# Kernel optimization log

Hardware: AMD Instinct MI355X
Metric: run time of the kernel (lower is better)

The kernel has to match this reference:

```python
import jax, jax.numpy as jnp
import numpy as np

D, H, W = 160, 192, 160


def _grid_sample_3d(vol, grid):
    """torch F.grid_sample (3D, bilinear/trilinear, padding='zeros', align_corners=False).
    vol: [B,C,D,H,W]; grid: [B,Do,Ho,Wo,3], last dim ordered (x,y,z) in [-1,1]."""
    B, C, Dv, Hv, Wv = vol.shape
    x, y, z = grid[..., 0], grid[..., 1], grid[..., 2]
    # align_corners=False unnormalization
    ix = ((x + 1.0) * Wv - 1.0) * 0.5
    iy = ((y + 1.0) * Hv - 1.0) * 0.5
    iz = ((z + 1.0) * Dv - 1.0) * 0.5
    fx, fy, fz = jnp.floor(ix), jnp.floor(iy), jnp.floor(iz)
    wx, wy, wz = ix - fx, iy - fy, iz - fz
    ix0, iy0, iz0 = fx.astype(jnp.int32), fy.astype(jnp.int32), fz.astype(jnp.int32)
    vol_flat = vol.reshape(B, C, Dv * Hv * Wv)
    out_sp = x.shape[1:]  # (Do, Ho, Wo)

    def gather(zi, yi, xi):
        inb = ((zi >= 0) & (zi < Dv) & (yi >= 0) & (yi < Hv) & (xi >= 0) & (xi < Wv))
        lin = ((jnp.clip(zi, 0, Dv - 1) * Hv + jnp.clip(yi, 0, Hv - 1)) * Wv
               + jnp.clip(xi, 0, Wv - 1)).reshape(B, -1)
        vals = jax.vmap(lambda v, i: v[:, i])(vol_flat, lin)  # [B,C,N]
        return vals.reshape((B, C) + out_sp) * inb[:, None].astype(vol.dtype)

    out = jnp.zeros((B, C) + tuple(out_sp), vol.dtype)
    # fixed 8-corner trilinear accumulation
    for dz, wz_ in ((0, 1.0 - wz), (1, wz)):
        for dy, wy_ in ((0, 1.0 - wy), (1, wy)):
            for dx, wx_ in ((0, 1.0 - wx), (1, wx)):
                w = (wz_ * wy_ * wx_)[:, None]  # [B,1,Do,Ho,Wo]
                out = out + w * gather(iz0 + dz, iy0 + dy, ix0 + dx)
    return out


def _voxel_grid():
    gd, gh, gw = jnp.meshgrid(jnp.arange(D, dtype=jnp.float32),
                              jnp.arange(H, dtype=jnp.float32),
                              jnp.arange(W, dtype=jnp.float32), indexing='ij')
    return jnp.stack([gd, gh, gw])[None]  # [1,3,D,H,W], channels (d,h,w)


def _to_xyz(t):
    # [B,3,D,H,W] channels (d,h,w) -> [B,D,H,W,3] channels (x,y,z)
    return jnp.moveaxis(t, 1, -1)[..., ::-1]


def setup_inputs() -> dict:
    key = jax.random.key(0)
    k1, k2, k3 = jax.random.split(key, 3)
    src = jax.random.normal(k1, (1, 1, D, H, W), dtype=jnp.float32)
    flow1 = jax.random.normal(k2, (1, 3, D, H, W), dtype=jnp.float32)
    flow2 = jax.random.normal(k3, (1, 3, D, H, W), dtype=jnp.float32)
    range_flow = jnp.float32(0.4)
    return {"src": src, "flow1": flow1, "flow2": flow2, "range_flow": range_flow}


def reference(src, flow1, flow2, range_flow):
    grid = _voxel_grid()  # voxel-coordinate identity grid
    # NOTE: grid2 is intentionally NOT normalized to [-1,1] (faithful to source quirk)
    grid2 = _to_xyz(grid + flow2 * range_flow)
    flow1_warped = _grid_sample_3d(flow1, grid2)
    out_flow = flow1_warped + flow2
    denom = jnp.array([D - 1, H - 1, W - 1], jnp.float32).reshape(1, 3, 1, 1, 1)
    new_locs_total = 2.0 * ((grid + out_flow * range_flow) / denom - 0.5)
    deform_2_img = _grid_sample_3d(src, _to_xyz(new_locs_total))
    return deform_2_img, out_flow
```

## Files before the change

kernel.cpp:

```cpp
#include <hip/hip_runtime.h>

constexpr int Dv = 160, Hv = 192, Wv = 160;
constexpr int NN = Dv * Hv * Wv;

constexpr int TW = 32, TH = 8, TD = 8;
constexpr int SX = 40, SY = 13, SZ = 13;
constexpr int SLEN = SX * SY * SZ;
constexpr int SVEC = SLEN / 4;
constexpr int SITER = (SVEC + 255) / 256;
constexpr int SPAD = SITER * 256 * 4;

__device__ __forceinline__ void tri3_rare(const float* __restrict__ v,
                                          float gx, float gy, float gz,
                                          float& o0, float& o1, float& o2) {
  o0 = 0.0f; o1 = 0.0f; o2 = 0.0f;
  float ix = ((gx + 1.0f) * (float)Wv - 1.0f) * 0.5f;
  float iy = ((gy + 1.0f) * (float)Hv - 1.0f) * 0.5f;
  float iz = ((gz + 1.0f) * (float)Dv - 1.0f) * 0.5f;
  float fx = floorf(ix), fy = floorf(iy), fz = floorf(iz);
  int x0 = (int)fx, y0 = (int)fy, z0 = (int)fz;
  if (x0 < -1 || x0 >= Wv || y0 < -1 || y0 >= Hv || z0 < -1 || z0 >= Dv)
    return;
  float wx = ix - fx, wy = iy - fy, wz = iz - fz;
#pragma unroll
  for (int c = 0; c < 8; ++c) {
    const int dz = (c >> 2) & 1, dy = (c >> 1) & 1, dx = c & 1;
    int zi = z0 + dz, yi = y0 + dy, xi = x0 + dx;
    if ((unsigned)zi < (unsigned)Dv && (unsigned)yi < (unsigned)Hv &&
        (unsigned)xi < (unsigned)Wv) {
      float wgt = (dz ? wz : 1.0f - wz) * (dy ? wy : 1.0f - wy) *
                  (dx ? wx : 1.0f - wx);
      int lin = (zi * Hv + yi) * Wv + xi;
      o0 += wgt * v[lin];
      o1 += wgt * v[NN + lin];
      o2 += wgt * v[2 * NN + lin];
    }
  }
}

__global__ __launch_bounds__(256)
void st_tiled_kernel(const float* __restrict__ src,
                     const float* __restrict__ flow1,
                     const float* __restrict__ flow2,
                     const float* __restrict__ rfp,
                     float* __restrict__ out) {
  __shared__ float tile[SPAD];

  const int tid = threadIdx.x;
  const int bx0 = blockIdx.x * TW;
  const int by0 = blockIdx.y * TH;
  const int bz0 = blockIdx.z * TD;
  const float rf = rfp[0];

  const int lx = tid & 7;
  const int ly = (tid >> 3) & 7;
  const int lz = tid >> 6;
  const int w0 = bx0 + lx * 4;
  const int h = by0 + ly;

  float4 f2d4[2], f2h4[2], f2w4[2];
#pragma unroll
  for (int s = 0; s < 2; ++s) {
    int d = bz0 + 2 * lz + s;
    int idx = (d * Hv + h) * Wv + w0;
    f2d4[s] = *(const float4*)(flow2 + idx);
    f2h4[s] = *(const float4*)(flow2 + NN + idx);
    f2w4[s] = *(const float4*)(flow2 + 2 * NN + idx);
  }

  const int bxo = bx0 - 4, byo = by0 - 2, bzo = bz0 - 2;
#pragma unroll
  for (int i = 0; i < SITER; ++i) {
    int t = tid + i * 256;
    int tt = (i == SITER - 1) ? min(t, SVEC - 1) : t;
    int e = tt * 4;
    int tz = e / (SY * SX);
    int r = e - tz * (SY * SX);
    int ty = r / SX;
    int tx = r - ty * SX;
    int gx = min(max(bxo + tx, 0), Wv - 4);
    int gy = min(max(byo + ty, 0), Hv - 1);
    int gz = min(max(bzo + tz, 0), Dv - 1);
    int g = (gz * Hv + gy) * Wv + gx;
    __builtin_amdgcn_global_load_lds(
        (const __attribute__((address_space(1))) void*)(src + g),
        (__attribute__((address_space(3))) void*)(tile + e), 16, 0, 0);
  }
  __syncthreads();

  const float hf = (float)h;
  constexpr float KX = (float)Wv / (float)(Wv - 1);
  constexpr float KY = (float)Hv / (float)(Hv - 1);
  constexpr float KZ = (float)Dv / (float)(Dv - 1);

#pragma unroll
  for (int s = 0; s < 2; ++s) {
    const int d = bz0 + 2 * lz + s;
    const float df = (float)d;
    const int idx = (d * Hv + h) * Wv + w0;

    float4 def, ofd4, ofh4, ofw4;
#pragma unroll
    for (int j = 0; j < 4; ++j) {
      const float wf = (float)(w0 + j);
      const float f2dv = (&f2d4[s].x)[j];
      const float f2hv = (&f2h4[s].x)[j];
      const float f2wv = (&f2w4[s].x)[j];

      float a0, a1, a2;
      tri3_rare(flow1, wf + rf * f2wv, hf + rf * f2hv, df + rf * f2dv,
                a0, a1, a2);

      float of_d = a0 + f2dv;
      float of_h = a1 + f2hv;
      float of_w = a2 + f2wv;
      (&ofd4.x)[j] = of_d;
      (&ofh4.x)[j] = of_h;
      (&ofw4.x)[j] = of_w;

      float ix = (wf + rf * of_w) * KX - 0.5f;
      float iy = (hf + rf * of_h) * KY - 0.5f;
      float iz = (df + rf * of_d) * KZ - 0.5f;

      float fx = floorf(ix), fy = floorf(iy), fz = floorf(iz);
      float wx = ix - fx, wy = iy - fy, wz = iz - fz;
      int x0 = (int)fx, y0 = (int)fy, z0 = (int)fz;

      float wx0 = ((unsigned)x0 < (unsigned)Wv) ? (1.0f - wx) : 0.0f;
      float wx1 = ((unsigned)(x0 + 1) < (unsigned)Wv) ? wx : 0.0f;
      float wy0 = ((unsigned)y0 < (unsigned)Hv) ? (1.0f - wy) : 0.0f;
      float wy1 = ((unsigned)(y0 + 1) < (unsigned)Hv) ? wy : 0.0f;
      float wz0 = ((unsigned)z0 < (unsigned)Dv) ? (1.0f - wz) : 0.0f;
      float wz1 = ((unsigned)(z0 + 1) < (unsigned)Dv) ? wz : 0.0f;

      int txi = x0 - bxo, tyi = y0 - byo, tzi = z0 - bzo;
      bool fast = ((unsigned)txi <= (unsigned)(SX - 2)) &
                  ((unsigned)tyi <= (unsigned)(SY - 2)) &
                  ((unsigned)tzi <= (unsigned)(SZ - 2));

      float v000, v001, v010, v011, v100, v101, v110, v111;
      if (fast) {
        int base = (tzi * SY + tyi) * SX + txi;
        v000 = tile[base];
        v001 = tile[base + 1];
        v010 = tile[base + SX];
        v011 = tile[base + SX + 1];
        v100 = tile[base + SY * SX];
        v101 = tile[base + SY * SX + 1];
        v110 = tile[base + SY * SX + SX];
        v111 = tile[base + SY * SX + SX + 1];
      } else {
        int xa0 = min(max(x0, 0), Wv - 1), xa1 = min(max(x0 + 1, 0), Wv - 1);
        int ya0 = min(max(y0, 0), Hv - 1), ya1 = min(max(y0 + 1, 0), Hv - 1);
        int za0 = min(max(z0, 0), Dv - 1), za1 = min(max(z0 + 1, 0), Dv - 1);
        int r00 = (za0 * Hv + ya0) * Wv;
        int r01 = (za0 * Hv + ya1) * Wv;
        int r10 = (za1 * Hv + ya0) * Wv;
        int r11 = (za1 * Hv + ya1) * Wv;
        v000 = src[r00 + xa0]; v001 = src[r00 + xa1];
        v010 = src[r01 + xa0]; v011 = src[r01 + xa1];
        v100 = src[r10 + xa0]; v101 = src[r10 + xa1];
        v110 = src[r11 + xa0]; v111 = src[r11 + xa1];
      }

      float c00 = v000 * wx0 + v001 * wx1;
      float c01 = v010 * wx0 + v011 * wx1;
      float c10 = v100 * wx0 + v101 * wx1;
      float c11 = v110 * wx0 + v111 * wx1;
      float c0 = c00 * wy0 + c01 * wy1;
      float c1 = c10 * wy0 + c11 * wy1;
      (&def.x)[j] = c0 * wz0 + c1 * wz1;
    }

    *(float4*)(out + idx) = def;
    *(float4*)(out + NN + idx) = ofd4;
    *(float4*)(out + 2 * NN + idx) = ofh4;
    *(float4*)(out + 3 * NN + idx) = ofw4;
  }
}

extern "C" void kernel_launch(void* const* d_in, const int* in_sizes, int n_in,
                              void* d_out, int out_size, void* d_ws, size_t ws_size,
                              hipStream_t stream) {
  const float* src   = (const float*)d_in[0];
  const float* flow1 = (const float*)d_in[1];
  const float* flow2 = (const float*)d_in[2];
  const float* rfp   = (const float*)d_in[3];
  float* out = (float*)d_out;

  dim3 grid(Wv / TW, Hv / TH, Dv / TD);
  hipLaunchKernelGGL(st_tiled_kernel, grid, dim3(256), 0, stream,
                     src, flow1, flow2, rfp, out);
}
```

Before: 179.4 us.

## Tile full W rows in LDS to remove x-halo and x-bound fast-path check

Each block now covers a full 160-wide row span (8 H by 4 D) and stages the whole x-extent of the src halo into LDS, so x-halo redundancy disappears and the fast path only checks y/z bounds. Each thread processes 5 float4 groups instead of 2, with all flow2 loads issued before the LDS barrier to overlap with the tile load. LDS per block grows to about 75 KB and the grid shrinks to 960 blocks, which lowers occupancy and may reduce latency hiding. The z-halo ratio worsens (9 planes staged for 4 output planes).

```diff
diff --git a/kernel.cpp b/kernel.cpp
--- a/kernel.cpp
+++ b/kernel.cpp
@@ -3,12 +3,16 @@
 constexpr int Dv = 160, Hv = 192, Wv = 160;
 constexpr int NN = Dv * Hv * Wv;
 
-constexpr int TW = 32, TH = 8, TD = 8;
-constexpr int SX = 40, SY = 13, SZ = 13;
+constexpr int TW = 160, TH = 8, TD = 4;
+constexpr int SX = 160, SY = 13, SZ = 9;
 constexpr int SLEN = SX * SY * SZ;
 constexpr int SVEC = SLEN / 4;
 constexpr int SITER = (SVEC + 255) / 256;
 constexpr int SPAD = SITER * 256 * 4;
+constexpr int SROW = SX / 4;
+constexpr int SPLANE = SY * SROW;
+constexpr int NG = TW * TH * TD / 4;
+constexpr int KSTEPS = NG / 256;
 
 __device__ __forceinline__ void tri3_rare(const float* __restrict__ v,
                                           float gx, float gy, float gz,
@@ -39,73 +43,76 @@
 }
 
 __global__ __launch_bounds__(256)
-void st_tiled_kernel(const float* __restrict__ src,
-                     const float* __restrict__ flow1,
-                     const float* __restrict__ flow2,
-                     const float* __restrict__ rfp,
-                     float* __restrict__ out) {
+void st_rowtile_kernel(const float* __restrict__ src,
+                       const float* __restrict__ flow1,
+                       const float* __restrict__ flow2,
+                       const float* __restrict__ rfp,
+                       float* __restrict__ out) {
   __shared__ float tile[SPAD];
 
   const int tid = threadIdx.x;
-  const int bx0 = blockIdx.x * TW;
   const int by0 = blockIdx.y * TH;
   const int bz0 = blockIdx.z * TD;
   const float rf = rfp[0];
 
-  const int lx = tid & 7;
-  const int ly = (tid >> 3) & 7;
-  const int lz = tid >> 6;
-  const int w0 = bx0 + lx * 4;
-  const int h = by0 + ly;
-
-  float4 f2d4[2], f2h4[2], f2w4[2];
-#pragma unroll
-  for (int s = 0; s < 2; ++s) {
-    int d = bz0 + 2 * lz + s;
-    int idx = (d * Hv + h) * Wv + w0;
-    f2d4[s] = *(const float4*)(flow2 + idx);
-    f2h4[s] = *(const float4*)(flow2 + NN + idx);
-    f2w4[s] = *(const float4*)(flow2 + 2 * NN + idx);
-  }
-
-  const int bxo = bx0 - 4, byo = by0 - 2, bzo = bz0 - 2;
+  const int byo = by0 - 2, bzo = bz0 - 2;
 #pragma unroll
   for (int i = 0; i < SITER; ++i) {
-    int t = tid + i * 256;
-    int tt = (i == SITER - 1) ? min(t, SVEC - 1) : t;
-    int e = tt * 4;
-    int tz = e / (SY * SX);
-    int r = e - tz * (SY * SX);
-    int ty = r / SX;
-    int tx = r - ty * SX;
-    int gx = min(max(bxo + tx, 0), Wv - 4);
+    int s = tid + i * 256;
+    s = (i == SITER - 1) ? min(s, SVEC - 1) : s;
+    int tz = s / SPLANE;
+    int r = s - tz * SPLANE;
+    int ty = r / SROW;
+    int tx4 = (r - ty * SROW) * 4;
     int gy = min(max(byo + ty, 0), Hv - 1);
     int gz = min(max(bzo + tz, 0), Dv - 1);
-    int g = (gz * Hv + gy) * Wv + gx;
+    int g = (gz * Hv + gy) * Wv + tx4;
     __builtin_amdgcn_global_load_lds(
         (const __attribute__((address_space(1))) void*)(src + g),
-        (__attribute__((address_space(3))) void*)(tile + e), 16, 0, 0);
+        (__attribute__((address_space(3))) void*)(tile + s * 4), 16, 0, 0);
+  }
+
+  int idxK[KSTEPS], wK[KSTEPS];
+  float dfK[KSTEPS], hfK[KSTEPS];
+#pragma unroll
+  for (int k = 0; k < KSTEPS; ++k) {
+    int g = tid + k * 256;
+    int dzl = g / (TH * SROW);
+    int rem = g - dzl * (TH * SROW);
+    int hl = rem / SROW;
+    int wg = (rem - hl * SROW) * 4;
+    int d = bz0 + dzl, h = by0 + hl;
+    wK[k] = wg;
+    dfK[k] = (float)d;
+    hfK[k] = (float)h;
+    idxK[k] = (d * Hv + h) * Wv + wg;
+  }
+  float4 f2d4[KSTEPS], f2h4[KSTEPS], f2w4[KSTEPS];
+#pragma unroll
+  for (int k = 0; k < KSTEPS; ++k) {
+    f2d4[k] = *(const float4*)(flow2 + idxK[k]);
+    f2h4[k] = *(const float4*)(flow2 + NN + idxK[k]);
+    f2w4[k] = *(const float4*)(flow2 + 2 * NN + idxK[k]);
   }
   __syncthreads();
 
-  const float hf = (float)h;
   constexpr float KX = (float)Wv / (float)(Wv - 1);
   constexpr float KY = (float)Hv / (float)(Hv - 1);
   constexpr float KZ = (float)Dv / (float)(Dv - 1);
 
 #pragma unroll
-  for (int s = 0; s < 2; ++s) {
-    const int d = bz0 + 2 * lz + s;
-    const float df = (float)d;
-    const int idx = (d * Hv + h) * Wv + w0;
+  for (int k = 0; k < KSTEPS; ++k) {
+    const float df = dfK[k];
+    const float hf = hfK[k];
+    const int idx = idxK[k];
 
     float4 def, ofd4, ofh4, ofw4;
 #pragma unroll
     for (int j = 0; j < 4; ++j) {
-      const float wf = (float)(w0 + j);
-      const float f2dv = (&f2d4[s].x)[j];
-      const float f2hv = (&f2h4[s].x)[j];
-      const float f2wv = (&f2w4[s].x)[j];
+      const float wf = (float)(wK[k] + j);
+      const float f2dv = (&f2d4[k].x)[j];
+      const float f2hv = (&f2h4[k].x)[j];
+      const float f2wv = (&f2w4[k].x)[j];
 
       float a0, a1, a2;
       tri3_rare(flow1, wf + rf * f2wv, hf + rf * f2hv, df + rf * f2dv,
@@ -133,24 +140,24 @@
       float wz0 = ((unsigned)z0 < (unsigned)Dv) ? (1.0f - wz) : 0.0f;
       float wz1 = ((unsigned)(z0 + 1) < (unsigned)Dv) ? wz : 0.0f;
 
-      int txi = x0 - bxo, tyi = y0 - byo, tzi = z0 - bzo;
-      bool fast = ((unsigned)txi <= (unsigned)(SX - 2)) &
-                  ((unsigned)tyi <= (unsigned)(SY - 2)) &
+      int xa0 = min(max(x0, 0), Wv - 1), xa1 = min(max(x0 + 1, 0), Wv - 1);
+
+      int tyi = y0 - byo, tzi = z0 - bzo;
+      bool fast = ((unsigned)tyi <= (unsigned)(SY - 2)) &
                   ((unsigned)tzi <= (unsigned)(SZ - 2));
 
       float v000, v001, v010, v011, v100, v101, v110, v111;
       if (fast) {
-        int base = (tzi * SY + tyi) * SX + txi;
-        v000 = tile[base];
-        v001 = tile[base + 1];
-        v010 = tile[base + SX];
-        v011 = tile[base + SX + 1];
-        v100 = tile[base + SY * SX];
-        v101 = tile[base + SY * SX + 1];
-        v110 = tile[base + SY * SX + SX];
-        v111 = tile[base + SY * SX + SX + 1];
+        int rb = (tzi * SY + tyi) * SX;
+        v000 = tile[rb + xa0];
+        v001 = tile[rb + xa1];
+        v010 = tile[rb + SX + xa0];
+        v011 = tile[rb + SX + xa1];
+        v100 = tile[rb + SY * SX + xa0];
+        v101 = tile[rb + SY * SX + xa1];
+        v110 = tile[rb + SY * SX + SX + xa0];
+        v111 = tile[rb + SY * SX + SX + xa1];
       } else {
-        int xa0 = min(max(x0, 0), Wv - 1), xa1 = min(max(x0 + 1, 0), Wv - 1);
         int ya0 = min(max(y0, 0), Hv - 1), ya1 = min(max(y0 + 1, 0), Hv - 1);
         int za0 = min(max(z0, 0), Dv - 1), za1 = min(max(z0 + 1, 0), Dv - 1);
         int r00 = (za0 * Hv + ya0) * Wv;
@@ -188,7 +195,7 @@
   const float* rfp   = (const float*)d_in[3];
   float* out = (float*)d_out;
 
-  dim3 grid(Wv / TW, Hv / TH, Dv / TD);
-  hipLaunchKernelGGL(st_tiled_kernel, grid, dim3(256), 0, stream,
+  dim3 grid(1, Hv / TH, Dv / TD);
+  hipLaunchKernelGGL(st_rowtile_kernel, grid, dim3(256), 0, stream,
                      src, flow1, flow2, rfp, out);
 }
```

Result: no change. 181.1 us (+1.0%).
